# Kernel optimization log

Hardware: AMD Instinct MI355X
Metric: run time of the kernel (lower is better)

Reference implementation:

```python
import jax, jax.numpy as jnp
import numpy as np

DISTANCE_EPS = 0.1


def setup_inputs() -> dict:
    key = jax.random.key(0)
    k1, k2, k3 = jax.random.split(key, 3)
    B, N, K, A = 2, 2048, 48, 4
    X = jax.random.normal(k1, (B, N, A, 3), dtype=jnp.float32)
    edge_idx = jax.random.randint(k2, (B, N, K), 0, N)
    C = jax.random.randint(k3, (B, N), 0, 4)
    return {"X": X, "edge_idx": edge_idx, "C": C}


def _normed_vec(V, eps=DISTANCE_EPS):
    # normalize with smoothing eps added to squared magnitude
    return V / jnp.sqrt((V * V).sum(-1, keepdims=True) + eps)


def reference(X, edge_idx, C):
    B, N, K = edge_idx.shape
    A = X.shape[2]
    X_flat = X.reshape(B, N, A * 3)
    batch = jnp.arange(B)[:, None, None]

    # Edge2mers: gather neighbor coords and concat with self coords
    X_j = X_flat[batch, edge_idx]                                   # (B,N,K,3A)
    X_i = jnp.broadcast_to(X_flat[:, :, None, :], (B, N, K, A * 3))  # (B,N,K,3A)
    X_ij = jnp.concatenate([X_i, X_j], -1).reshape(B, N, K, 2 * A, 3)

    mask_i = (C > 0).astype(jnp.float32)[..., None]   # (B,N,1)
    mask_j = mask_i[batch, edge_idx]                  # (B,N,K,1)
    mask_ij = mask_i[:, :, None, :] * mask_j          # (B,N,K,1)

    # pairwise normalized difference vectors: [a,b] = X_ij[b] - X_ij[a]
    U_ij = _normed_vec(X_ij[:, :, :, None, :, :] - X_ij[:, :, :, :, None, :])  # (B,N,K,2A,2A,3)

    # per-residue backbone frame from N, CA, C atoms
    X_N, X_CA, X_Cc = X[:, :, 0], X[:, :, 1], X[:, :, 2]
    u_CA_N = _normed_vec(X_N - X_CA)
    u_CA_C = _normed_vec(X_Cc - X_CA)
    n_1 = u_CA_N
    n_2 = _normed_vec(jnp.cross(n_1, u_CA_C))
    n_3 = _normed_vec(jnp.cross(n_1, n_2))
    R = jnp.stack([n_1, n_2, n_3], -1)  # (B,N,3,3)

    # rotate each pairwise vector into the local frame of residue i
    U_rot = jnp.einsum('nijabx,nixy->nijaby', U_ij, R)
    feature_ij = U_rot.reshape(B, N, K, -1)           # (B,N,K,3*(2A)^2)
    edge_h = mask_ij * feature_ij
    return edge_h
```

## Files before the change

### kernel.cpp

```cpp
#include <hip/hip_runtime.h>


constexpr int Bq = 2, Nq = 2048, Kq = 48;
constexpr float EPS = 0.1f;

struct F3 { float x, y, z; };
__device__ __forceinline__ F3 f3sub(F3 a, F3 b) { return {a.x - b.x, a.y - b.y, a.z - b.z}; }
__device__ __forceinline__ float f3dot(F3 a, F3 b) {
    return fmaf(a.x, b.x, fmaf(a.y, b.y, a.z * b.z));
}
__device__ __forceinline__ F3 f3scale(F3 a, float s) { return {a.x * s, a.y * s, a.z * s}; }
__device__ __forceinline__ F3 f3normed(F3 v) {
    float inv = rsqrtf(f3dot(v, v) + EPS);
    return f3scale(v, inv);
}
__device__ __forceinline__ F3 f3cross(F3 a, F3 b) {
    return {a.y * b.z - a.z * b.y, a.z * b.x - a.x * b.z, a.x * b.y - a.y * b.x};
}

__global__ __launch_bounds__(256) void edge_orient_v3_kernel(
    const float* __restrict__ X,
    const int* __restrict__ E,
    const int* __restrict__ C,
    float* __restrict__ out)
{
    __shared__ float4 smem[2048];

    const int t = threadIdx.x;
    const unsigned edge = blockIdx.x * 32u + (unsigned)(t >> 3);
    const unsigned a = t & 7u;

    const unsigned node = edge / (unsigned)Kq;
    const unsigned bidx = node >> 11;
    const int j = E[edge];
    const unsigned nodej = (bidx << 11) + (unsigned)j;

    const float m = (C[node] > 0 && C[nodej] > 0) ? 1.0f : 0.0f;

    const float4* Xi4 = reinterpret_cast<const float4*>(X + (size_t)node * 12);
    const float4* Xj4 = reinterpret_cast<const float4*>(X + (size_t)nodej * 12);
    const float4 A0 = Xi4[0], A1 = Xi4[1], A2 = Xi4[2];
    const float4 B0 = Xj4[0], B1 = Xj4[1], B2 = Xj4[2];

    const F3 p0 = {A0.x, A0.y, A0.z};
    const F3 p1 = {A0.w, A1.x, A1.y};
    const F3 p2 = {A1.z, A1.w, A2.x};
    const F3 p3 = {A2.y, A2.z, A2.w};
    const F3 p4 = {B0.x, B0.y, B0.z};
    const F3 p5 = {B0.w, B1.x, B1.y};
    const F3 p6 = {B1.z, B1.w, B2.x};
    const F3 p7 = {B2.y, B2.z, B2.w};

    const F3 n1u = f3normed(f3sub(p0, p1));
    const F3 uC  = f3normed(f3sub(p2, p1));
    const F3 n2u = f3normed(f3cross(n1u, uC));
    const F3 n3u = f3normed(f3cross(n1u, n2u));
    const F3 n1 = f3scale(n1u, m), n2 = f3scale(n2u, m), n3 = f3scale(n3u, m);

    const float* pap = X + (size_t)(a < 4u ? node : nodej) * 12 + (a & 3u) * 3;
    const F3 pa = {pap[0], pap[1], pap[2]};

    float o[24] __attribute__((aligned(16)));
#pragma unroll
    for (int b2 = 0; b2 < 8; ++b2) {
        F3 pb;
        switch (b2) {
            case 0: pb = p0; break; case 1: pb = p1; break;
            case 2: pb = p2; break; case 3: pb = p3; break;
            case 4: pb = p4; break; case 5: pb = p5; break;
            case 6: pb = p6; break; default: pb = p7; break;
        }
        const F3 d = f3sub(pb, pa);
        const float nn = fmaf(d.x, d.x, fmaf(d.y, d.y, fmaf(d.z, d.z, EPS)));
        const float inv = rsqrtf(nn);
        o[b2 * 3 + 0] = f3dot(d, n1) * inv;
        o[b2 * 3 + 1] = f3dot(d, n2) * inv;
        o[b2 * 3 + 2] = f3dot(d, n3) * inv;
    }

    const float4* ov = reinterpret_cast<const float4*>(o);
#pragma unroll
    for (int i = 0; i < 6; ++i) {
        smem[t * 8 + (i ^ (t & 7))] = ov[i];
    }
    __syncthreads();

    float4* outb = reinterpret_cast<float4*>(out) + (size_t)blockIdx.x * 1536;
#pragma unroll
    for (int s = 0; s < 6; ++s) {
        const unsigned g4 = (unsigned)s * 256u + (unsigned)t;
        const unsigned o4 = g4 / 6u;
        const unsigned i4 = g4 - o4 * 6u;
        outb[g4] = smem[o4 * 8u + (i4 ^ (o4 & 7u))];
    }
}

extern "C" void kernel_launch(void* const* d_in, const int* in_sizes, int n_in,
                              void* d_out, int out_size, void* d_ws, size_t ws_size,
                              hipStream_t stream) {
    const float* X = (const float*)d_in[0];
    const int*   E = (const int*)d_in[1];
    const int*   C = (const int*)d_in[2];
    float* out = (float*)d_out;

    const int total_edges = Bq * Nq * Kq;
    dim3 block(256);
    dim3 grid(total_edges / 32);
    edge_orient_v3_kernel<<<grid, block, 0, stream>>>(X, E, C, out);
}
```

Measured before the change: 29.47 us.

## Split each row across two threads, halve per-thread work, use nontemporal stores

Each (edge, a) output row is now computed by two threads, one covering the i-residue atoms and one the j-residue atoms. This gives 16 edges per block and doubles the grid. The shared-memory staging becomes a smaller contiguous layout without the XOR swizzle, and the global writes use nontemporal stores. The aim is more parallelism, lower register pressure and less cache pollution from the large write-only output. The cost is duplicated frame computation and index loads per thread, plus possible LDS bank conflicts from the stride-3 writes.

Result: no change. 29.72 us (+0.9%).

```diff
diff --git a/kernel.cpp b/kernel.cpp
--- a/kernel.cpp
+++ b/kernel.cpp
@@ -3,6 +3,8 @@
 
 constexpr int Bq = 2, Nq = 2048, Kq = 48;
 constexpr float EPS = 0.1f;
+
+typedef float vf4 __attribute__((ext_vector_type(4)));
 
 struct F3 { float x, y, z; };
 __device__ __forceinline__ F3 f3sub(F3 a, F3 b) { return {a.x - b.x, a.y - b.y, a.z - b.z}; }
@@ -18,17 +20,19 @@
     return {a.y * b.z - a.z * b.y, a.z * b.x - a.x * b.z, a.x * b.y - a.y * b.x};
 }
 
-__global__ __launch_bounds__(256) void edge_orient_v3_kernel(
+__global__ __launch_bounds__(256) void edge_orient_v4_kernel(
     const float* __restrict__ X,
     const int* __restrict__ E,
     const int* __restrict__ C,
     float* __restrict__ out)
 {
-    __shared__ float4 smem[2048];
+    __shared__ vf4 smem[768];
 
     const int t = threadIdx.x;
-    const unsigned edge = blockIdx.x * 32u + (unsigned)(t >> 3);
-    const unsigned a = t & 7u;
+    const unsigned edge = blockIdx.x * 16u + (unsigned)(t >> 4);
+    const unsigned sub  = t & 15u;
+    const unsigned a    = sub >> 1;
+    const unsigned half = sub & 1u;
 
     const unsigned node = edge / (unsigned)Kq;
     const unsigned bidx = node >> 11;
@@ -37,61 +41,55 @@
 
     const float m = (C[node] > 0 && C[nodej] > 0) ? 1.0f : 0.0f;
 
-    const float4* Xi4 = reinterpret_cast<const float4*>(X + (size_t)node * 12);
-    const float4* Xj4 = reinterpret_cast<const float4*>(X + (size_t)nodej * 12);
-    const float4 A0 = Xi4[0], A1 = Xi4[1], A2 = Xi4[2];
-    const float4 B0 = Xj4[0], B1 = Xj4[1], B2 = Xj4[2];
+    const vf4* Xi4 = reinterpret_cast<const vf4*>(X + (size_t)node * 12);
+    const vf4* Xj4 = reinterpret_cast<const vf4*>(X + (size_t)nodej * 12);
+    const vf4 A0 = Xi4[0], A1 = Xi4[1], A2 = Xi4[2];
 
     const F3 p0 = {A0.x, A0.y, A0.z};
     const F3 p1 = {A0.w, A1.x, A1.y};
     const F3 p2 = {A1.z, A1.w, A2.x};
-    const F3 p3 = {A2.y, A2.z, A2.w};
-    const F3 p4 = {B0.x, B0.y, B0.z};
-    const F3 p5 = {B0.w, B1.x, B1.y};
-    const F3 p6 = {B1.z, B1.w, B2.x};
-    const F3 p7 = {B2.y, B2.z, B2.w};
-
     const F3 n1u = f3normed(f3sub(p0, p1));
     const F3 uC  = f3normed(f3sub(p2, p1));
     const F3 n2u = f3normed(f3cross(n1u, uC));
     const F3 n3u = f3normed(f3cross(n1u, n2u));
     const F3 n1 = f3scale(n1u, m), n2 = f3scale(n2u, m), n3 = f3scale(n3u, m);
 
+    const vf4* Pb4 = half ? Xj4 : Xi4;
+    const vf4 Q0 = Pb4[0], Q1 = Pb4[1], Q2 = Pb4[2];
+    const F3 q0 = {Q0.x, Q0.y, Q0.z};
+    const F3 q1 = {Q0.w, Q1.x, Q1.y};
+    const F3 q2 = {Q1.z, Q1.w, Q2.x};
+    const F3 q3 = {Q2.y, Q2.z, Q2.w};
+
     const float* pap = X + (size_t)(a < 4u ? node : nodej) * 12 + (a & 3u) * 3;
     const F3 pa = {pap[0], pap[1], pap[2]};
 
-    float o[24] __attribute__((aligned(16)));
+    float o[12] __attribute__((aligned(16)));
 #pragma unroll
-    for (int b2 = 0; b2 < 8; ++b2) {
+    for (int k = 0; k < 4; ++k) {
         F3 pb;
-        switch (b2) {
-            case 0: pb = p0; break; case 1: pb = p1; break;
-            case 2: pb = p2; break; case 3: pb = p3; break;
-            case 4: pb = p4; break; case 5: pb = p5; break;
-            case 6: pb = p6; break; default: pb = p7; break;
+        switch (k) {
+            case 0: pb = q0; break; case 1: pb = q1; break;
+            case 2: pb = q2; break; default: pb = q3; break;
         }
         const F3 d = f3sub(pb, pa);
         const float nn = fmaf(d.x, d.x, fmaf(d.y, d.y, fmaf(d.z, d.z, EPS)));
         const float inv = rsqrtf(nn);
-        o[b2 * 3 + 0] = f3dot(d, n1) * inv;
-        o[b2 * 3 + 1] = f3dot(d, n2) * inv;
-        o[b2 * 3 + 2] = f3dot(d, n3) * inv;
+        o[k * 3 + 0] = f3dot(d, n1) * inv;
+        o[k * 3 + 1] = f3dot(d, n2) * inv;
+        o[k * 3 + 2] = f3dot(d, n3) * inv;
     }
 
-    const float4* ov = reinterpret_cast<const float4*>(o);
+    const vf4* ov = reinterpret_cast<const vf4*>(o);
 #pragma unroll
-    for (int i = 0; i < 6; ++i) {
-        smem[t * 8 + (i ^ (t & 7))] = ov[i];
-    }
+    for (int i = 0; i < 3; ++i) smem[3 * t + i] = ov[i];
     __syncthreads();
 
-    float4* outb = reinterpret_cast<float4*>(out) + (size_t)blockIdx.x * 1536;
+    vf4* outb = reinterpret_cast<vf4*>(out) + (size_t)blockIdx.x * 768;
 #pragma unroll
-    for (int s = 0; s < 6; ++s) {
-        const unsigned g4 = (unsigned)s * 256u + (unsigned)t;
-        const unsigned o4 = g4 / 6u;
-        const unsigned i4 = g4 - o4 * 6u;
-        outb[g4] = smem[o4 * 8u + (i4 ^ (o4 & 7u))];
+    for (int s = 0; s < 3; ++s) {
+        const int g = s * 256 + t;
+        __builtin_nontemporal_store(smem[g], &outb[g]);
     }
 }
 
@@ -105,6 +103,6 @@
 
     const int total_edges = Bq * Nq * Kq;
     dim3 block(256);
-    dim3 grid(total_edges / 32);
-    edge_orient_v3_kernel<<<grid, block, 0, stream>>>(X, E, C, out);
+    dim3 grid(total_edges / 16);
+    edge_orient_v4_kernel<<<grid, block, 0, stream>>>(X, E, C, out);
 }
```
